# Performance work log

Measured on AMD Instinct MI355X. Metric: run time of the kernel, lower is better.

## Reference

```python
import jax, jax.numpy as jnp
import numpy as np

N = 100000       # nodes
E = 3200000      # edges (avg degree 32)
IN_C = 64        # in_channels
OUT_C = 10       # out_channels
F = 32           # hidden width of every GCNConv
L = 31           # number of GCNConv layers


def setup_inputs() -> dict:
    key = jax.random.key(0)
    ks = jax.random.split(key, 6)
    x = jax.random.normal(ks[0], (N, IN_C), dtype=jnp.float32)
    edge_index = jax.random.randint(ks[1], (2, E), 0, N, dtype=jnp.int64)
    W1 = jax.random.normal(ks[2], (IN_C, F), dtype=jnp.float32) * 0.1
    b1 = jnp.zeros((F,), dtype=jnp.float32)
    Wc = jax.random.normal(ks[3], (L, F, F), dtype=jnp.float32) * 0.1
    bc = jnp.zeros((L, F), dtype=jnp.float32)
    W2 = jax.random.normal(ks[4], (32 * F, OUT_C), dtype=jnp.float32) * 0.05
    b2 = jnp.zeros((OUT_C,), dtype=jnp.float32)
    return {"x": x, "edge_index": edge_index, "W1": W1, "b1": b1,
            "Wc": Wc, "bc": bc, "W2": W2, "b2": b2}


def mynorm(t):
    mn = t.min(axis=1, keepdims=True)
    mx = t.max(axis=1, keepdims=True)
    return 2.0 * (t - mn) / (mx - mn + 1e-8) - 1.0


def reference(x, edge_index, W1, b1, Wc, bc, W2, b2):
    src, dst = edge_index[0], edge_index[1]
    # GCN symmetric normalization with self-loops: deg = in-degree + 1
    deg = jax.ops.segment_sum(jnp.ones((E,), jnp.float32), dst, num_segments=N) + 1.0
    dis = jax.lax.rsqrt(deg)                       # [N]
    enorm = (dis[src] * dis[dst])[:, None]         # per-edge norm
    snorm = (dis * dis)[:, None]                   # self-loop norm

    def gcn(h, W, b):
        h = h @ W                                  # [N,32]
        agg = jax.ops.segment_sum(h[src] * enorm, dst, num_segments=N)
        return agg + snorm * h + b

    x0 = mynorm(jax.nn.relu(x @ W1 + b1))
    xs = [x0]
    for i in range(L):
        xs.append(gcn(xs[-1], Wc[i], bc[i]))
    norms = [mynorm(t) for t in xs]
    parts = [x0, xs[1]]                            # x0 and xx1 = x1 (raw)
    for i in range(2, 32):
        # quirk in original: index 16 uses raw x16, not a norm difference
        parts.append(xs[16] if i == 16 else norms[i] - norms[i - 2])
    feats = jnp.concatenate(parts, axis=1)         # [N, 32*32]
    return feats @ W2 + b2
```

## Files before the change

### kernel.cpp

```cpp
#include <hip/hip_runtime.h>


#define NB 4
#define BSHIFT 15
#define CSH 9

__device__ __forceinline__ float shflx(float v, int m) { return __shfl_xor(v, m, 64); }

__global__ __launch_bounds__(256) void k_chist(const int* __restrict__ dst, int E,
                                               int* __restrict__ gcnt, int G1) {
    __shared__ int lh[256];
    lh[threadIdx.x] = 0;
    __syncthreads();
    int chunk = (E + gridDim.x - 1) / gridDim.x;
    int s0 = blockIdx.x * chunk, s1 = min(E, s0 + chunk);
    for (int e = s0 + threadIdx.x; e < s1; e += 256)
        atomicAdd(&lh[dst[e] >> CSH], 1);
    __syncthreads();
    if (threadIdx.x < G1 && lh[threadIdx.x])
        atomicAdd(&gcnt[threadIdx.x], lh[threadIdx.x]);
}

__global__ void k_cscan(const int* __restrict__ gcnt, int* __restrict__ gptr,
                        int* __restrict__ gcur, int G1, int E) {
    __shared__ int s[256];
    int t = threadIdx.x;
    int v = (t < G1) ? gcnt[t] : 0;
    s[t] = v;
    __syncthreads();
    for (int off = 1; off < 256; off <<= 1) {
        int tv = (t >= off) ? s[t - off] : 0;
        __syncthreads();
        s[t] += tv;
        __syncthreads();
    }
    if (t < G1) { int ex = s[t] - v; gptr[t] = ex; gcur[t] = ex; }
    if (t == 0) gptr[G1] = E;
}

__global__ __launch_bounds__(256) void k_cscatter(const int* __restrict__ src,
                                                  const int* __restrict__ dst, int E,
                                                  int* __restrict__ gcur,
                                                  int* __restrict__ tmp, int G1) {
    __shared__ int lh[256], lc[256];
    lh[threadIdx.x] = 0;
    __syncthreads();
    int chunk = (E + gridDim.x - 1) / gridDim.x;
    int s0 = blockIdx.x * chunk, s1 = min(E, s0 + chunk);
    for (int e = s0 + threadIdx.x; e < s1; e += 256)
        atomicAdd(&lh[dst[e] >> CSH], 1);
    __syncthreads();
    if (threadIdx.x < G1) {
        int c = lh[threadIdx.x];
        lc[threadIdx.x] = c ? atomicAdd(&gcur[threadIdx.x], c) : 0;
    }
    __syncthreads();
    for (int e = s0 + threadIdx.x; e < s1; e += 256) {
        int d = dst[e];
        int pos = atomicAdd(&lc[d >> CSH], 1);
        tmp[pos] = src[e] | ((d & ((1 << CSH) - 1)) << 17);
    }
}

__global__ __launch_bounds__(256) void k_build(const int* __restrict__ tmp,
                                               const int* __restrict__ gptr,
                                               int* __restrict__ rp4,
                                               int* __restrict__ csr,
                                               float* __restrict__ dis,
                                               int N, int M) {
    __shared__ int h[2048];
    __shared__ int c[2048];
    __shared__ int s[256];
    int g = blockIdx.x;
    int gb = gptr[g], ge = gptr[g + 1];
    int t = threadIdx.x;
#pragma unroll
    for (int k = 0; k < 8; ++k) h[t * 8 + k] = 0;
    __syncthreads();
    for (int e = gb + t; e < ge; e += 256) {
        int w = tmp[e];
        int srcv = w & 0x1FFFF, ldst = w >> 17;
        atomicAdd(&h[ldst * NB + (srcv >> BSHIFT)], 1);
    }
    __syncthreads();
    int base8 = t * 8;
    int loc[8], sum = 0;
#pragma unroll
    for (int k = 0; k < 8; ++k) { loc[k] = h[base8 + k]; sum += loc[k]; }
    s[t] = sum;
    __syncthreads();
    for (int off = 1; off < 256; off <<= 1) {
        int tv = (t >= off) ? s[t - off] : 0;
        __syncthreads();
        s[t] += tv;
        __syncthreads();
    }
    int run = s[t] - sum;
    int rowbase = g * 2048;
#pragma unroll
    for (int k = 0; k < 8; ++k) {
        int i = base8 + k;
        c[i] = run;
        int ig = rowbase + i;
        if (ig <= M) rp4[ig] = gb + run;
        run += loc[k];
    }
    __syncthreads();
    for (int e = gb + t; e < ge; e += 256) {
        int w = tmp[e];
        int srcv = w & 0x1FFFF, ldst = w >> 17;
        int pos = atomicAdd(&c[ldst * NB + (srcv >> BSHIFT)], 1);
        csr[gb + pos] = srcv;
    }
    int nodebase = g << CSH;
    for (int ln = t; ln < (1 << CSH); ln += 256) {
        int n = nodebase + ln;
        if (n < N) {
            int d = h[ln * NB] + h[ln * NB + 1] + h[ln * NB + 2] + h[ln * NB + 3];
            dis[n] = rsqrtf((float)d + 1.0f);
        }
    }
    if (g == gridDim.x - 1 && t == 0) rp4[M] = ge;
}

__global__ void k_mnorm(const float* __restrict__ W2, float* __restrict__ Mn,
                        float* __restrict__ Rw, float* __restrict__ C0) {
    int idx = blockIdx.x * blockDim.x + threadIdx.x;
    if (idx >= 32 * 32 * 10) return;
    int c = idx % 32, o = (idx / 32) % 10, j = idx / 320;
    float v = 0.f;
    if (j >= 2 && j != 16) v += W2[(32 * j + c) * 10 + o];
    if (j <= 29 && j != 14) v -= W2[(32 * (j + 2) + c) * 10 + o];
    Mn[idx] = v;
    float rw = (j == 0 || j == 1 || j == 16) ? W2[(32 * j + c) * 10 + o] : 0.f;
    Rw[idx] = rw;
    if (j == 0) C0[idx] = v + rw;
}

__global__ __launch_bounds__(256) void k_x0(
    const float* __restrict__ x, const float* __restrict__ W1, const float* __restrict__ b1,
    const float* __restrict__ b2, const float* __restrict__ C0,
    const float* __restrict__ dis, float* __restrict__ hs, float* __restrict__ out, int N)
{
    __shared__ float Wt[32 * 68];
    __shared__ float xs[8 * 64];
    __shared__ float bs[32];
    __shared__ float Cs[10 * 36];
    __shared__ float xmat[8 * 36];
    int t = threadIdx.x;
    for (int i = t; i < 2048; i += 256) {
        int k = i >> 5, cc = i & 31;
        Wt[cc * 68 + k] = W1[i];
    }
    for (int i = t; i < 320; i += 256) {
        int o = i >> 5, cc = i & 31;
        Cs[o * 36 + cc] = C0[i];
    }
    if (t < 32) bs[t] = b1[t];
    int base = blockIdx.x * 8;
    {
        int nf2 = (min(N - base, 8)) * 32;
        const float2* x2 = (const float2*)(x + (size_t)base * 64);
        float2* xs2 = (float2*)xs;
        for (int i = t; i < nf2; i += 256) xs2[i] = x2[i];
    }
    __syncthreads();

    int node8 = t >> 5, c = t & 31;
    int n = base + node8;
    bool nvalid = (n < N);

    const float4* xs4 = (const float4*)(xs + node8 * 64);
    const float4* Wt4 = (const float4*)(Wt + c * 68);
    float acc = bs[c];
#pragma unroll
    for (int k4 = 0; k4 < 16; ++k4) {
        float4 xv = xs4[k4];
        float4 wv = Wt4[k4];
        acc += xv.x * wv.x + xv.y * wv.y + xv.z * wv.z + xv.w * wv.w;
    }
    acc = fmaxf(acc, 0.f);

    float mn = acc, mx = acc;
#pragma unroll
    for (int m = 1; m <= 16; m <<= 1) { mn = fminf(mn, shflx(mn, m)); mx = fmaxf(mx, shflx(mx, m)); }
    float x0 = 2.f * (acc - mn) / (mx - mn + 1e-8f) - 1.f;
    if (nvalid) {
        float dn = dis[n];
        hs[(size_t)n * 32 + c] = dn * x0;
        xmat[node8 * 36 + c] = x0;
    }
    __syncthreads();

    if (t < 80) {
        int n8 = t / 10, o = t - n8 * 10;
        int no = base + n8;
        if (no < N) {
            const float4* xr = (const float4*)(xmat + n8 * 36);
            const float4* cr = (const float4*)(Cs + o * 36);
            float a = 0.f;
#pragma unroll
            for (int k = 0; k < 8; ++k) {
                float4 xv = xr[k];
                float4 cv = cr[k];
                a += xv.x * cv.x + xv.y * cv.y + xv.z * cv.z + xv.w * cv.w;
            }
            out[(size_t)no * 10 + o] = b2[o] + a;
        }
    }
}

__global__ __launch_bounds__(256) void k_gcn(
    const float4* __restrict__ hs_in, float4* __restrict__ hs_out,
    const float* __restrict__ dis, const int* __restrict__ rp4,
    const int* __restrict__ csr,
    const float* __restrict__ W, const float* __restrict__ b,
    const float* __restrict__ Mn, const float* __restrict__ Rw,
    float* __restrict__ out, int N, int israw)
{
    __shared__ float Ws[1024];
    __shared__ float bs[32];
    __shared__ float Ms[320];
    __shared__ float Rs[320];
    for (int i = threadIdx.x; i < 1024; i += 256) Ws[i] = W[i];
    for (int i = threadIdx.x; i < 320; i += 256) { Ms[i] = Mn[i]; Rs[i] = Rw[i]; }
    if (threadIdx.x < 32) bs[threadIdx.x] = b[threadIdx.x];
    __syncthreads();

    int lane = threadIdx.x & 63;
    int q = lane & 7;
    int i8 = lane >> 3;
    int wave = threadIdx.x >> 6;
    int n = blockIdx.x * 32 + wave * 8 + i8;
    bool valid = (n < N);
    int nn = valid ? n : (N - 1);

    float4 acc = hs_in[(size_t)nn * 8 + q];

    int rbase = nn * NB;
    int rs = rp4[rbase];
    for (int p = 0; p < NB; ++p) {
        int re = rp4[rbase + p + 1];
        int e = rs;
        for (; e + 3 < re; e += 4) {
            int s0 = csr[e], s1 = csr[e + 1], s2 = csr[e + 2], s3 = csr[e + 3];
            float4 v0 = hs_in[(size_t)s0 * 8 + q];
            float4 v1 = hs_in[(size_t)s1 * 8 + q];
            float4 v2 = hs_in[(size_t)s2 * 8 + q];
            float4 v3 = hs_in[(size_t)s3 * 8 + q];
            acc.x += v0.x; acc.y += v0.y; acc.z += v0.z; acc.w += v0.w;
            acc.x += v1.x; acc.y += v1.y; acc.z += v1.z; acc.w += v1.w;
            acc.x += v2.x; acc.y += v2.y; acc.z += v2.z; acc.w += v2.w;
            acc.x += v3.x; acc.y += v3.y; acc.z += v3.z; acc.w += v3.w;
        }
        if (e + 1 < re) {
            int s0 = csr[e], s1 = csr[e + 1];
            float4 v0 = hs_in[(size_t)s0 * 8 + q];
            float4 v1 = hs_in[(size_t)s1 * 8 + q];
            acc.x += v0.x; acc.y += v0.y; acc.z += v0.z; acc.w += v0.w;
            acc.x += v1.x; acc.y += v1.y; acc.z += v1.z; acc.w += v1.w;
            e += 2;
        }
        if (e < re) {
            int s0 = csr[e];
            float4 v0 = hs_in[(size_t)s0 * 8 + q];
            acc.x += v0.x; acc.y += v0.y; acc.z += v0.z; acc.w += v0.w;
        }
        rs = re;
        __syncthreads();
    }

    float dn = dis[nn];
    float4 g = make_float4(dn * acc.x, dn * acc.y, dn * acc.z, dn * acc.w);

    const float4* W4 = (const float4*)Ws;
    float4 bb = ((const float4*)bs)[q];
    float4 xn = bb;
    int ibase = lane & 0x38;
#pragma unroll
    for (int kp = 0; kp < 8; ++kp) {
        int sl = ibase | kp;
        float gx = __shfl(g.x, sl, 64);
        float gy = __shfl(g.y, sl, 64);
        float gz = __shfl(g.z, sl, 64);
        float gw = __shfl(g.w, sl, 64);
        float4 w0 = W4[(kp * 4 + 0) * 8 + q];
        float4 w1 = W4[(kp * 4 + 1) * 8 + q];
        float4 w2 = W4[(kp * 4 + 2) * 8 + q];
        float4 w3 = W4[(kp * 4 + 3) * 8 + q];
        xn.x += gx * w0.x + gy * w1.x + gz * w2.x + gw * w3.x;
        xn.y += gx * w0.y + gy * w1.y + gz * w2.y + gw * w3.y;
        xn.z += gx * w0.z + gy * w1.z + gz * w2.z + gw * w3.z;
        xn.w += gx * w0.w + gy * w1.w + gz * w2.w + gw * w3.w;
    }

    if (valid)
        hs_out[(size_t)n * 8 + q] = make_float4(dn * xn.x, dn * xn.y, dn * xn.z, dn * xn.w);

    float mn = fminf(fminf(xn.x, xn.y), fminf(xn.z, xn.w));
    float mx = fmaxf(fmaxf(xn.x, xn.y), fmaxf(xn.z, xn.w));
#pragma unroll
    for (int m = 1; m <= 4; m <<= 1) { mn = fminf(mn, shflx(mn, m)); mx = fmaxf(mx, shflx(mx, m)); }
    float sc = 2.f / (mx - mn + 1e-8f);
    float4 nr = make_float4((xn.x - mn) * sc - 1.f, (xn.y - mn) * sc - 1.f,
                            (xn.z - mn) * sc - 1.f, (xn.w - mn) * sc - 1.f);

    const float4* M4 = (const float4*)Ms;
    const float4* R4 = (const float4*)Rs;
    float outA = 0.f, outB = 0.f;
#pragma unroll
    for (int o = 0; o < 10; ++o) {
        float4 m4 = M4[o * 8 + q];
        float t = nr.x * m4.x + nr.y * m4.y + nr.z * m4.z + nr.w * m4.w;
        if (israw) {
            float4 r4 = R4[o * 8 + q];
            t += xn.x * r4.x + xn.y * r4.y + xn.z * r4.z + xn.w * r4.w;
        }
        t += shflx(t, 1); t += shflx(t, 2); t += shflx(t, 4);
        if (o == q) outA = t;
        if (o == 8 + q) outB = t;
    }
    if (valid) {
        out[n * 10 + q] += outA;
        if (q < 2) out[n * 10 + 8 + q] += outB;
    }
}

extern "C" void kernel_launch(void* const* d_in, const int* in_sizes, int n_in,
                              void* d_out, int out_size, void* d_ws, size_t ws_size,
                              hipStream_t stream)
{
    const float* x  = (const float*)d_in[0];
    const int*   ei = (const int*)d_in[1];
    const float* W1 = (const float*)d_in[2];
    const float* b1 = (const float*)d_in[3];
    const float* Wc = (const float*)d_in[4];
    const float* bc = (const float*)d_in[5];
    const float* W2 = (const float*)d_in[6];
    const float* b2 = (const float*)d_in[7];
    float* out = (float*)d_out;

    const int N = in_sizes[0] / 64;
    const int E = in_sizes[1] / 2;
    const int M = N * NB;
    const int G1 = (N + (1 << CSH) - 1) >> CSH;
    const int* src = ei;
    const int* dst = ei + E;

    char* ws = (char*)d_ws;
    size_t off = 0;
    auto alloc = [&](size_t bytes) -> void* {
        void* p = ws + off;
        off = (off + bytes + 255) & ~size_t(255);
        return p;
    };
    int*   gcnt    = (int*)alloc(256 * 4);
    int*   gptr    = (int*)alloc(257 * 4);
    int*   gcur    = (int*)alloc(256 * 4);
    int*   rp4     = (int*)alloc((size_t)(M + 1) * 4);
    float* dis     = (float*)alloc((size_t)N * 4);
    int*   tmp     = (int*)alloc((size_t)E * 4);
    int*   csr     = (int*)alloc((size_t)E * 4);
    float* hs_a    = (float*)alloc((size_t)N * 32 * 4);
    float* hs_b    = (float*)alloc((size_t)N * 32 * 4);
    float* Mn      = (float*)alloc(32 * 32 * 10 * 4);
    float* Rw      = (float*)alloc(32 * 32 * 10 * 4);
    float* C0      = (float*)alloc(320 * 4);

    hipMemsetAsync(gcnt, 0, 256 * 4, stream);
    k_chist<<<256, 256, 0, stream>>>(dst, E, gcnt, G1);
    k_cscan<<<1, 256, 0, stream>>>(gcnt, gptr, gcur, G1, E);
    k_cscatter<<<256, 256, 0, stream>>>(src, dst, E, gcur, tmp, G1);
    k_build<<<G1, 256, 0, stream>>>(tmp, gptr, rp4, csr, dis, N, M);
    k_mnorm<<<(32 * 32 * 10 + 255) / 256, 256, 0, stream>>>(W2, Mn, Rw, C0);

    const int gb0 = (N + 7) / 8;
    k_x0<<<gb0, 256, 0, stream>>>(x, W1, b1, b2, C0, dis, hs_a, out, N);

    const int gb = (N + 31) / 32;
    float* hin = hs_a; float* hout = hs_b;
    for (int j = 1; j <= 31; ++j) {
        int israw = (j == 1 || j == 16) ? 1 : 0;
        k_gcn<<<gb, 256, 0, stream>>>((const float4*)hin, (float4*)hout, dis, rp4,
                                      csr,
                                      Wc + (size_t)(j - 1) * 1024,
                                      bc + (size_t)(j - 1) * 32,
                                      Mn + (size_t)j * 320,
                                      Rw + (size_t)j * 320,
                                      out, N, israw);
        float* t = hin; hin = hout; hout = t;
    }
}
```

Baseline: 2.055 ms.

## Pad CSR buckets to multiples of four with dummy zero node for int4 index loads

Each source-bucket segment in the CSR is padded up to a multiple of four entries, and the padding is filled with a dummy node index N whose feature row is kept at zero in both ping-pong buffers. The aggregation loop then reads indices as int4 with one-ahead prefetch and drops the two-and-one remainder tails, removing scalar index loads and branches. The cost is padding writes during graph build, extra gathers of the zero row, and a per-group slack region plus a gend array to locate segment ends.

```diff
diff --git a/kernel.cpp b/kernel.cpp
--- a/kernel.cpp
+++ b/kernel.cpp
@@ -4,6 +4,7 @@
 #define NB 4
 #define BSHIFT 15
 #define CSH 9
+#define GSLACK 6152
 
 __device__ __forceinline__ float shflx(float v, int m) { return __shfl_xor(v, m, 64); }
 
@@ -67,12 +68,14 @@
                                                int* __restrict__ rp4,
                                                int* __restrict__ csr,
                                                float* __restrict__ dis,
+                                               int* __restrict__ gend,
                                                int N, int M) {
     __shared__ int h[2048];
     __shared__ int c[2048];
     __shared__ int s[256];
     int g = blockIdx.x;
     int gb = gptr[g], ge = gptr[g + 1];
+    int gbP = ((gb + 3) & ~3) + g * GSLACK;
     int t = threadIdx.x;
 #pragma unroll
     for (int k = 0; k < 8; ++k) h[t * 8 + k] = 0;
@@ -84,10 +87,10 @@
     }
     __syncthreads();
     int base8 = t * 8;
-    int loc[8], sum = 0;
-#pragma unroll
-    for (int k = 0; k < 8; ++k) { loc[k] = h[base8 + k]; sum += loc[k]; }
-    s[t] = sum;
+    int loc[8], sumP = 0;
+#pragma unroll
+    for (int k = 0; k < 8; ++k) { loc[k] = h[base8 + k]; sumP += (loc[k] + 3) & ~3; }
+    s[t] = sumP;
     __syncthreads();
     for (int off = 1; off < 256; off <<= 1) {
         int tv = (t >= off) ? s[t - off] : 0;
@@ -95,22 +98,26 @@
         s[t] += tv;
         __syncthreads();
     }
-    int run = s[t] - sum;
+    int runP = s[t] - sumP;
     int rowbase = g * 2048;
 #pragma unroll
     for (int k = 0; k < 8; ++k) {
         int i = base8 + k;
-        c[i] = run;
+        int abs0 = gbP + runP;
+        c[i] = abs0;
         int ig = rowbase + i;
-        if (ig <= M) rp4[ig] = gb + run;
-        run += loc[k];
-    }
+        if (ig <= M) rp4[ig] = abs0;
+        int lp = (loc[k] + 3) & ~3;
+        for (int j = loc[k]; j < lp; ++j) csr[abs0 + j] = N;
+        runP += lp;
+    }
+    if (t == 0) gend[g] = 0;
     __syncthreads();
     for (int e = gb + t; e < ge; e += 256) {
         int w = tmp[e];
         int srcv = w & 0x1FFFF, ldst = w >> 17;
         int pos = atomicAdd(&c[ldst * NB + (srcv >> BSHIFT)], 1);
-        csr[gb + pos] = srcv;
+        csr[pos] = srcv;
     }
     int nodebase = g << CSH;
     for (int ln = t; ln < (1 << CSH); ln += 256) {
@@ -120,7 +127,8 @@
             dis[n] = rsqrtf((float)d + 1.0f);
         }
     }
-    if (g == gridDim.x - 1 && t == 0) rp4[M] = ge;
+    if (t == 0) gend[g] = gbP + s[255];
+    if (g == gridDim.x - 1 && t == 0) rp4[M] = gbP + s[255];
 }
 
 __global__ void k_mnorm(const float* __restrict__ W2, float* __restrict__ Mn,
@@ -157,6 +165,7 @@
         Cs[o * 36 + cc] = C0[i];
     }
     if (t < 32) bs[t] = b1[t];
+    if (blockIdx.x == 0 && t < 32) hs[(size_t)N * 32 + t] = 0.f;
     int base = blockIdx.x * 8;
     {
         int nf2 = (min(N - base, 8)) * 32;
@@ -213,7 +222,7 @@
 __global__ __launch_bounds__(256) void k_gcn(
     const float4* __restrict__ hs_in, float4* __restrict__ hs_out,
     const float* __restrict__ dis, const int* __restrict__ rp4,
-    const int* __restrict__ csr,
+    const int* __restrict__ csr, const int* __restrict__ gend,
     const float* __restrict__ W, const float* __restrict__ b,
     const float* __restrict__ Mn, const float* __restrict__ Rw,
     float* __restrict__ out, int N, int israw)
@@ -225,6 +234,8 @@
     for (int i = threadIdx.x; i < 1024; i += 256) Ws[i] = W[i];
     for (int i = threadIdx.x; i < 320; i += 256) { Ms[i] = Mn[i]; Rs[i] = Rw[i]; }
     if (threadIdx.x < 32) bs[threadIdx.x] = b[threadIdx.x];
+    if (blockIdx.x == 0 && threadIdx.x < 8)
+        hs_out[(size_t)N * 8 + threadIdx.x] = make_float4(0.f, 0.f, 0.f, 0.f);
     __syncthreads();
 
     int lane = threadIdx.x & 63;
@@ -239,32 +250,23 @@
 
     int rbase = nn * NB;
     int rs = rp4[rbase];
+    int e3 = ((nn & ((1 << CSH) - 1)) == ((1 << CSH) - 1)) ? gend[nn >> CSH]
+                                                          : rp4[rbase + 4];
+    const int4* csr4 = (const int4*)csr;
+    int4 idx = csr4[rs >> 2];
     for (int p = 0; p < NB; ++p) {
-        int re = rp4[rbase + p + 1];
-        int e = rs;
-        for (; e + 3 < re; e += 4) {
-            int s0 = csr[e], s1 = csr[e + 1], s2 = csr[e + 2], s3 = csr[e + 3];
-            float4 v0 = hs_in[(size_t)s0 * 8 + q];
-            float4 v1 = hs_in[(size_t)s1 * 8 + q];
-            float4 v2 = hs_in[(size_t)s2 * 8 + q];
-            float4 v3 = hs_in[(size_t)s3 * 8 + q];
+        int re = (p == NB - 1) ? e3 : rp4[rbase + p + 1];
+        for (int e = rs; e < re; e += 4) {
+            int s0 = idx.x, s1 = idx.y, s2 = idx.z, s3 = idx.w;
+            idx = csr4[(e + 4) >> 2];
+            float4 v0 = hs_in[(size_t)(s0 * 8 + q)];
+            float4 v1 = hs_in[(size_t)(s1 * 8 + q)];
+            float4 v2 = hs_in[(size_t)(s2 * 8 + q)];
+            float4 v3 = hs_in[(size_t)(s3 * 8 + q)];
             acc.x += v0.x; acc.y += v0.y; acc.z += v0.z; acc.w += v0.w;
             acc.x += v1.x; acc.y += v1.y; acc.z += v1.z; acc.w += v1.w;
             acc.x += v2.x; acc.y += v2.y; acc.z += v2.z; acc.w += v2.w;
             acc.x += v3.x; acc.y += v3.y; acc.z += v3.z; acc.w += v3.w;
-        }
-        if (e + 1 < re) {
-            int s0 = csr[e], s1 = csr[e + 1];
-            float4 v0 = hs_in[(size_t)s0 * 8 + q];
-            float4 v1 = hs_in[(size_t)s1 * 8 + q];
-            acc.x += v0.x; acc.y += v0.y; acc.z += v0.z; acc.w += v0.w;
-            acc.x += v1.x; acc.y += v1.y; acc.z += v1.z; acc.w += v1.w;
-            e += 2;
-        }
-        if (e < re) {
-            int s0 = csr[e];
-            float4 v0 = hs_in[(size_t)s0 * 8 + q];
-            acc.x += v0.x; acc.y += v0.y; acc.z += v0.z; acc.w += v0.w;
         }
         rs = re;
         __syncthreads();
@@ -359,10 +361,11 @@
     int*   gcur    = (int*)alloc(256 * 4);
     int*   rp4     = (int*)alloc((size_t)(M + 1) * 4);
     float* dis     = (float*)alloc((size_t)N * 4);
+    int*   gend    = (int*)alloc(256 * 4);
     int*   tmp     = (int*)alloc((size_t)E * 4);
-    int*   csr     = (int*)alloc((size_t)E * 4);
-    float* hs_a    = (float*)alloc((size_t)N * 32 * 4);
-    float* hs_b    = (float*)alloc((size_t)N * 32 * 4);
+    int*   csr     = (int*)alloc(((size_t)E + (size_t)G1 * GSLACK + 64) * 4);
+    float* hs_a    = (float*)alloc((size_t)(N + 1) * 32 * 4);
+    float* hs_b    = (float*)alloc((size_t)(N + 1) * 32 * 4);
     float* Mn      = (float*)alloc(32 * 32 * 10 * 4);
     float* Rw      = (float*)alloc(32 * 32 * 10 * 4);
     float* C0      = (float*)alloc(320 * 4);
@@ -371,7 +374,7 @@
     k_chist<<<256, 256, 0, stream>>>(dst, E, gcnt, G1);
     k_cscan<<<1, 256, 0, stream>>>(gcnt, gptr, gcur, G1, E);
     k_cscatter<<<256, 256, 0, stream>>>(src, dst, E, gcur, tmp, G1);
-    k_build<<<G1, 256, 0, stream>>>(tmp, gptr, rp4, csr, dis, N, M);
+    k_build<<<G1, 256, 0, stream>>>(tmp, gptr, rp4, csr, dis, gend, N, M);
     k_mnorm<<<(32 * 32 * 10 + 255) / 256, 256, 0, stream>>>(W2, Mn, Rw, C0);
 
     const int gb0 = (N + 7) / 8;
@@ -382,7 +385,7 @@
     for (int j = 1; j <= 31; ++j) {
         int israw = (j == 1 || j == 16) ? 1 : 0;
         k_gcn<<<gb, 256, 0, stream>>>((const float4*)hin, (float4*)hout, dis, rp4,
-                                      csr,
+                                      csr, gend,
                                       Wc + (size_t)(j - 1) * 1024,
                                       bc + (size_t)(j - 1) * 32,
                                       Mn + (size_t)j * 320,
```

New measurement: 1.893 ms. 1.09x faster.
